# Optimization experiments

Hardware: AMD Instinct MI355X
Metric: run time of the kernel (lower is better)

## Reference

```python
import jax, jax.numpy as jnp
import numpy as np


def setup_inputs() -> dict:
    key = jax.random.key(0)
    k1, k2, k3 = jax.random.split(key, 3)
    B, H, S, D = 2, 8, 4096, 64
    queries = jax.random.normal(k1, (B, H, S, D), dtype=jnp.float32)
    keys = jax.random.normal(k2, (B, H, S, D), dtype=jnp.float32)
    values = jax.random.normal(k3, (B, H, S, D), dtype=jnp.float32)
    mask = jnp.zeros((1, 1, S, S), dtype=jnp.float32)
    return {"queries": queries, "keys": keys, "values": values, "d_k": D, "mask": mask}


def reference(queries, keys, values, d_k, mask):
    # scores: [B, H, Sq, Sk]
    scale = 1.0 / jnp.sqrt(jnp.asarray(d_k, dtype=queries.dtype))
    scores = jnp.einsum("bhqd,bhkd->bhqk", queries, keys) * scale
    scores = scores + (-1e9) * mask  # additive mask, broadcasts over B, H
    weights = jax.nn.softmax(scores, axis=-1)
    return jnp.einsum("bhqk,bhkd->bhqd", weights, values)
```

## Files before the change

### kernel.cpp

```cpp
#include <hip/hip_runtime.h>

#define S_LEN 4096
#define DHEAD 64
#define BQ    128
#define BK    64
#define NT    (S_LEN / BK)
#define KPAD  72
#define NBH   16
#define TILE_HALFS (BK * DHEAD)
#define WS_KV_HALFS ((size_t)NBH * NT * TILE_HALFS)

typedef __fp16   pk16x2 __attribute__((ext_vector_type(2)));
typedef _Float16 half4v __attribute__((ext_vector_type(4)));
typedef _Float16 half8  __attribute__((ext_vector_type(8)));
typedef float    f32x4  __attribute__((ext_vector_type(4)));

__device__ __forceinline__ void gl_lds16(const _Float16* g, _Float16* l) {
    __builtin_amdgcn_global_load_lds(
        (const __attribute__((address_space(1))) unsigned int*)g,
        (__attribute__((address_space(3))) unsigned int*)l, 16, 0, 0);
}

__global__ void mask_flag_kernel(const float4* __restrict__ mask, int* __restrict__ flag) {
    const long stride = 2048L * 256;
    long i = (long)blockIdx.x * 256 + threadIdx.x;
    int nz = 0;
    #pragma unroll
    for (int it = 0; it < 8; ++it) {
        float4 a = mask[i + it * stride];
        nz |= (a.x != 0.f) | (a.y != 0.f) | (a.z != 0.f) | (a.w != 0.f);
    }
    if (__any(nz)) {
        if ((threadIdx.x & 63) == 0) atomicOr(flag, 1);
    }
}

__global__ void conv_kernel(const float* __restrict__ Kg, const float* __restrict__ Vg,
                            const float* __restrict__ mask,
                            _Float16* __restrict__ wsK, _Float16* __restrict__ wsV,
                            int* __restrict__ flag) {
    const int tid  = threadIdx.x;
    const int tile = blockIdx.x;
    __shared__ __align__(16) _Float16 T[64][64];

    if (blockIdx.y == 0) {
        const float* Ksrc = Kg + (long)tile * TILE_HALFS;
        _Float16*    dst  = wsK + (long)tile * TILE_HALFS;
        #pragma unroll
        for (int it = 0; it < 2; ++it) {
            int m = tid + it * 256;
            int r = m >> 3, c = m & 7;
            const float4* s4 = (const float4*)(Ksrc + r * DHEAD + ((c ^ (r & 7)) << 3));
            float4 a = s4[0], b = s4[1];
            union { pk16x2 p[4]; half8 h; } u;
            u.p[0] = __builtin_amdgcn_cvt_pkrtz(a.x, a.y);
            u.p[1] = __builtin_amdgcn_cvt_pkrtz(a.z, a.w);
            u.p[2] = __builtin_amdgcn_cvt_pkrtz(b.x, b.y);
            u.p[3] = __builtin_amdgcn_cvt_pkrtz(b.z, b.w);
            *(half8*)(dst + m * 8) = u.h;
        }
    } else if (blockIdx.y == 1) {
        const float* Vsrc = Vg + (long)tile * TILE_HALFS;
        const int r  = tid >> 2;
        const int d0 = (tid & 3) << 4;
        const float4* s4 = (const float4*)(Vsrc + r * DHEAD + d0);
        float vv[16];
        *(float4*)&vv[0]  = s4[0];
        *(float4*)&vv[4]  = s4[1];
        *(float4*)&vv[8]  = s4[2];
        *(float4*)&vv[12] = s4[3];
        #pragma unroll
        for (int j = 0; j < 16; j += 2) {
            pk16x2 p = __builtin_amdgcn_cvt_pkrtz(vv[j], vv[j + 1]);
            T[d0 + j][r]     = *((_Float16*)&p);
            T[d0 + j + 1][r] = *((_Float16*)&p + 1);
        }
        __syncthreads();
        _Float16* dst = wsV + (long)tile * TILE_HALFS;
        #pragma unroll
        for (int it = 0; it < 2; ++it) {
            int m = tid + it * 256;
            int d = m >> 3, c = m & 7;
            *(half8*)(dst + m * 8) = *(const half8*)&T[d][(c ^ (d & 7)) << 3];
        }
    } else {
        const float4* m4 = (const float4*)mask;
        const long stride = 1024L * 256;
        long i = (long)blockIdx.x * 256 + tid;
        int nz = 0;
        #pragma unroll
        for (int it = 0; it < 16; ++it) {
            float4 a = m4[i + it * stride];
            nz |= (a.x != 0.f) | (a.y != 0.f) | (a.z != 0.f) | (a.w != 0.f);
        }
        if (__any(nz)) {
            if ((tid & 63) == 0) atomicOr(flag, 1);
        }
    }
}

__global__ __launch_bounds__(256, 2) void attn_ws_kernel(
    const float* __restrict__ Q, const _Float16* __restrict__ KW,
    const _Float16* __restrict__ VW, const int* __restrict__ dk,
    const float* __restrict__ mask, const int* __restrict__ maskflag,
    float* __restrict__ O)
{
    const int qt   = blockIdx.x;
    const int bh   = blockIdx.y;
    const int tid  = threadIdx.x;
    const int wave = tid >> 6;
    const int lane = tid & 63;
    const int l15  = lane & 15;
    const int quad = lane >> 4;
    const int sw   = (l15 & 7) << 3;
    const int rq8  = quad << 3;

    const long base = (long)bh * S_LEN * DHEAD;
    const float* Qh = Q + base;
    float*       Oh = O + base;
    const _Float16* gk = KW + (long)bh * (NT * TILE_HALFS);
    const _Float16* gv = VW + (long)bh * (NT * TILE_HALFS);

    const int q0 = qt * BQ + wave * 32;
    const float csq  = rsqrtf((float)dk[0]) * 1.44269504088896f;
    const float mfac = -1e9f * 1.44269504088896f;
    const bool use_mask = (maskflag[0] != 0);

    __shared__ __align__(16) _Float16 KT[2][TILE_HALFS];
    __shared__ __align__(16) _Float16 VT[2][TILE_HALFS];
    __shared__ __align__(16) _Float16 Pw[4][32][KPAD];

    half8 qf[2][2];
    #pragma unroll
    for (int f = 0; f < 2; ++f) {
        #pragma unroll
        for (int kc = 0; kc < 2; ++kc) {
            const float4* src = (const float4*)(Qh + (long)(q0 + f*16 + l15) * DHEAD + kc*32 + rq8);
            float4 a = src[0], b = src[1];
            union { pk16x2 p[4]; half8 h; } u;
            u.p[0] = __builtin_amdgcn_cvt_pkrtz(a.x*csq, a.y*csq);
            u.p[1] = __builtin_amdgcn_cvt_pkrtz(a.z*csq, a.w*csq);
            u.p[2] = __builtin_amdgcn_cvt_pkrtz(b.x*csq, b.y*csq);
            u.p[3] = __builtin_amdgcn_cvt_pkrtz(b.z*csq, b.w*csq);
            qf[f][kc] = u.h;
        }
    }

    auto stage = [&](int kt, int b) {
        const _Float16* k8 = gk + (long)kt * TILE_HALFS + tid * 8;
        const _Float16* v8 = gv + (long)kt * TILE_HALFS + tid * 8;
        gl_lds16(k8,        &KT[b][tid * 8]);
        gl_lds16(k8 + 2048, &KT[b][2048 + tid * 8]);
        gl_lds16(v8,        &VT[b][tid * 8]);
        gl_lds16(v8 + 2048, &VT[b][2048 + tid * 8]);
    };

    f32x4 o[2][4];
    #pragma unroll
    for (int f = 0; f < 2; ++f)
        #pragma unroll
        for (int dt = 0; dt < 4; ++dt) o[f][dt] = (f32x4){0.f, 0.f, 0.f, 0.f};
    float m_i[2] = {-INFINITY, -INFINITY};
    float l_i[2] = {0.0f, 0.0f};

    stage(0, 0);
    __syncthreads();

    for (int kt = 0; kt < NT; ++kt) {
        const int b = kt & 1;
        if (kt + 1 < NT) stage(kt + 1, b ^ 1);

        f32x4 st[2][4];
        #pragma unroll
        for (int f = 0; f < 2; ++f)
            #pragma unroll
            for (int nt = 0; nt < 4; ++nt) st[f][nt] = (f32x4){0.f,0.f,0.f,0.f};
        __builtin_amdgcn_s_setprio(1);
        #pragma unroll
        for (int nt = 0; nt < 4; ++nt) {
            const int rb = (nt << 10) + (l15 << 6);
            #pragma unroll
            for (int kc = 0; kc < 2; ++kc) {
                half8 af = *(const half8*)&KT[b][rb + ((kc*32 + rq8) ^ sw)];
                st[0][nt] = __builtin_amdgcn_mfma_f32_16x16x32_f16(af, qf[0][kc], st[0][nt], 0, 0, 0);
                st[1][nt] = __builtin_amdgcn_mfma_f32_16x16x32_f16(af, qf[1][kc], st[1][nt], 0, 0, 0);
            }
        }
        __builtin_amdgcn_s_setprio(0);

        if (use_mask) {
            #pragma unroll
            for (int f = 0; f < 2; ++f) {
                const long mrow = (long)(q0 + f*16 + l15) * S_LEN + kt*BK;
                #pragma unroll
                for (int nt = 0; nt < 4; ++nt)
                    #pragma unroll
                    for (int r = 0; r < 4; ++r)
                        st[f][nt][r] += mfac * mask[mrow + nt*16 + quad*4 + r];
            }
        }

        #pragma unroll
        for (int f = 0; f < 2; ++f) {
            float mx = fmaxf(fmaxf(fmaxf(st[f][0][0], st[f][0][1]), fmaxf(st[f][0][2], st[f][0][3])),
                             fmaxf(fmaxf(st[f][1][0], st[f][1][1]), fmaxf(st[f][1][2], st[f][1][3])));
            float mx2 = fmaxf(fmaxf(fmaxf(st[f][2][0], st[f][2][1]), fmaxf(st[f][2][2], st[f][2][3])),
                              fmaxf(fmaxf(st[f][3][0], st[f][3][1]), fmaxf(st[f][3][2], st[f][3][3])));
            mx = fmaxf(mx, mx2);
            mx = fmaxf(mx, __shfl_xor(mx, 16, 64));
            mx = fmaxf(mx, __shfl_xor(mx, 32, 64));
            const bool need = __any(mx > m_i[f]);
            const float mnew = need ? fmaxf(m_i[f], mx) : m_i[f];
            float rsum = 0.0f;
            #pragma unroll
            for (int nt = 0; nt < 4; ++nt) {
                #pragma unroll
                for (int r = 0; r < 4; ++r) {
                    float p = __builtin_amdgcn_exp2f(st[f][nt][r] - mnew);
                    st[f][nt][r] = p;
                    rsum += p;
                }
            }
            rsum += __shfl_xor(rsum, 16, 64);
            rsum += __shfl_xor(rsum, 32, 64);
            if (need) {
                const float alpha = __builtin_amdgcn_exp2f(m_i[f] - mnew);
                #pragma unroll
                for (int r = 0; r < 4; ++r) {
                    float a_r = __shfl(alpha, quad*4 + r, 64);
                    #pragma unroll
                    for (int dt = 0; dt < 4; ++dt) o[f][dt][r] *= a_r;
                }
                l_i[f] = alpha * l_i[f] + rsum;
                m_i[f] = mnew;
            } else {
                l_i[f] += rsum;
            }
        }

        #pragma unroll
        for (int f = 0; f < 2; ++f)
            #pragma unroll
            for (int nt = 0; nt < 4; ++nt) {
                union { pk16x2 p[2]; half4v h; } up;
                up.p[0] = __builtin_amdgcn_cvt_pkrtz(st[f][nt][0], st[f][nt][1]);
                up.p[1] = __builtin_amdgcn_cvt_pkrtz(st[f][nt][2], st[f][nt][3]);
                *(half4v*)&Pw[wave][f*16 + l15][nt*16 + quad*4] = up.h;
            }

        __builtin_amdgcn_s_setprio(1);
        #pragma unroll
        for (int kc2 = 0; kc2 < 2; ++kc2) {
            half8 pa0 = *(const half8*)&Pw[wave][l15][kc2*32 + rq8];
            half8 pa1 = *(const half8*)&Pw[wave][16 + l15][kc2*32 + rq8];
            #pragma unroll
            for (int dt = 0; dt < 4; ++dt) {
                const int db = (dt << 10) + (l15 << 6);
                half8 vb = *(const half8*)&VT[b][db + ((kc2*32 + rq8) ^ sw)];
                o[0][dt] = __builtin_amdgcn_mfma_f32_16x16x32_f16(pa0, vb, o[0][dt], 0, 0, 0);
                o[1][dt] = __builtin_amdgcn_mfma_f32_16x16x32_f16(pa1, vb, o[1][dt], 0, 0, 0);
            }
        }
        __builtin_amdgcn_s_setprio(0);

        if (kt + 1 < NT) __syncthreads();
    }

    #pragma unroll
    for (int f = 0; f < 2; ++f) {
        #pragma unroll
        for (int r = 0; r < 4; ++r) {
            float lq = __shfl(l_i[f], quad*4 + r, 64);
            float linv = __builtin_amdgcn_rcpf(lq);
            const long row = (long)(q0 + f*16 + quad*4 + r) * DHEAD;
            #pragma unroll
            for (int dt = 0; dt < 4; ++dt)
                Oh[row + dt*16 + l15] = o[f][dt][r] * linv;
        }
    }
}

__global__ __launch_bounds__(256, 2) void attn_kernel_fb(
    const float* __restrict__ Q, const float* __restrict__ K,
    const float* __restrict__ V, const int* __restrict__ dk,
    const float* __restrict__ mask, const int* __restrict__ maskflag,
    float* __restrict__ O)
{
    const int qt   = blockIdx.x;
    const int bh   = blockIdx.y;
    const int tid  = threadIdx.x;
    const int wave = tid >> 6;
    const int lane = tid & 63;
    const int l15  = lane & 15;
    const int quad = lane >> 4;

    const long base = (long)bh * S_LEN * DHEAD;
    const float* Qh = Q + base;
    const float* Kh = K + base;
    const float* Vh = V + base;
    float*       Oh = O + base;

    const int q0 = qt * BQ + wave * 32;
    const float csq  = rsqrtf((float)dk[0]) * 1.44269504088896f;
    const float mfac = -1e9f * 1.44269504088896f;
    const bool use_mask = (maskflag[0] != 0);

    __shared__ __align__(16) _Float16 Kt[2][BK][KPAD];
    __shared__ __align__(16) _Float16 Vt[2][DHEAD * KPAD];
    __shared__ __align__(16) _Float16 Pw[4][32][KPAD];

    half8 qf[2][2];
    #pragma unroll
    for (int f = 0; f < 2; ++f) {
        #pragma unroll
        for (int kc = 0; kc < 2; ++kc) {
            const float4* src = (const float4*)(Qh + (long)(q0 + f*16 + l15) * DHEAD + kc*32 + quad*8);
            float4 a = src[0], b = src[1];
            union { pk16x2 p[4]; half8 h; } u;
            u.p[0] = __builtin_amdgcn_cvt_pkrtz(a.x*csq, a.y*csq);
            u.p[1] = __builtin_amdgcn_cvt_pkrtz(a.z*csq, a.w*csq);
            u.p[2] = __builtin_amdgcn_cvt_pkrtz(b.x*csq, b.y*csq);
            u.p[3] = __builtin_amdgcn_cvt_pkrtz(b.z*csq, b.w*csq);
            qf[f][kc] = u.h;
        }
    }

    const int kr  = tid >> 2;
    const int ks  = tid & 3;
    const int vrp = tid >> 3;
    const int vdq = tid & 7;
    const float* Kb = Kh + (long)kr * DHEAD + ks * 16;
    const float* Vb = Vh + (long)(2 * vrp) * DHEAD + vdq * 8;
    const int vcol = (((vrp >> 2) ^ vdq) << 3) + ((2 * vrp) & 7);
    const int vd0  = vdq * 8;

    float4 kf[4], vf[4];
    auto load_tile = [&](int kt) {
        const float4* kp  = (const float4*)(Kb + (long)kt * BK * DHEAD);
        kf[0] = kp[0]; kf[1] = kp[1]; kf[2] = kp[2]; kf[3] = kp[3];
        const float4* vp0 = (const float4*)(Vb + (long)kt * BK * DHEAD);
        const float4* vp1 = (const float4*)(Vb + (long)kt * BK * DHEAD + DHEAD);
        vf[0] = vp0[0]; vf[1] = vp0[1]; vf[2] = vp1[0]; vf[3] = vp1[1];
    };
    auto store_tile = [&](int b) {
        union { pk16x2 p[4]; half8 h; } u0, u1;
        u0.p[0] = __builtin_amdgcn_cvt_pkrtz(kf[0].x, kf[0].y);
        u0.p[1] = __builtin_amdgcn_cvt_pkrtz(kf[0].z, kf[0].w);
        u0.p[2] = __builtin_amdgcn_cvt_pkrtz(kf[1].x, kf[1].y);
        u0.p[3] = __builtin_amdgcn_cvt_pkrtz(kf[1].z, kf[1].w);
        u1.p[0] = __builtin_amdgcn_cvt_pkrtz(kf[2].x, kf[2].y);
        u1.p[1] = __builtin_amdgcn_cvt_pkrtz(kf[2].z, kf[2].w);
        u1.p[2] = __builtin_amdgcn_cvt_pkrtz(kf[3].x, kf[3].y);
        u1.p[3] = __builtin_amdgcn_cvt_pkrtz(kf[3].z, kf[3].w);
        *(half8*)&Kt[b][kr][ks*16]     = u0.h;
        *(half8*)&Kt[b][kr][ks*16 + 8] = u1.h;
        _Float16* vt = &Vt[b][0];
        *(pk16x2*)&vt[(vd0+0)*KPAD + vcol] = __builtin_amdgcn_cvt_pkrtz(vf[0].x, vf[2].x);
        *(pk16x2*)&vt[(vd0+1)*KPAD + vcol] = __builtin_amdgcn_cvt_pkrtz(vf[0].y, vf[2].y);
        *(pk16x2*)&vt[(vd0+2)*KPAD + vcol] = __builtin_amdgcn_cvt_pkrtz(vf[0].z, vf[2].z);
        *(pk16x2*)&vt[(vd0+3)*KPAD + vcol] = __builtin_amdgcn_cvt_pkrtz(vf[0].w, vf[2].w);
        *(pk16x2*)&vt[(vd0+4)*KPAD + vcol] = __builtin_amdgcn_cvt_pkrtz(vf[1].x, vf[3].x);
        *(pk16x2*)&vt[(vd0+5)*KPAD + vcol] = __builtin_amdgcn_cvt_pkrtz(vf[1].y, vf[3].y);
        *(pk16x2*)&vt[(vd0+6)*KPAD + vcol] = __builtin_amdgcn_cvt_pkrtz(vf[1].z, vf[3].z);
        *(pk16x2*)&vt[(vd0+7)*KPAD + vcol] = __builtin_amdgcn_cvt_pkrtz(vf[1].w, vf[3].w);
    };

    f32x4 o[2][4];
    #pragma unroll
    for (int f = 0; f < 2; ++f)
        #pragma unroll
        for (int dt = 0; dt < 4; ++dt) o[f][dt] = (f32x4){0.f, 0.f, 0.f, 0.f};
    float m_i[2] = {-INFINITY, -INFINITY};
    float l_i[2] = {0.0f, 0.0f};

    load_tile(0);
    store_tile(0);
    __syncthreads();

    for (int kt = 0; kt < NT; ++kt) {
        const int b = kt & 1;
        if (kt + 1 < NT) load_tile(kt + 1);

        f32x4 st[2][4];
        #pragma unroll
        for (int f = 0; f < 2; ++f)
            #pragma unroll
            for (int nt = 0; nt < 4; ++nt) st[f][nt] = (f32x4){0.f,0.f,0.f,0.f};
        #pragma unroll
        for (int nt = 0; nt < 4; ++nt) {
            #pragma unroll
            for (int kc = 0; kc < 2; ++kc) {
                half8 af = *(const half8*)&Kt[b][nt*16 + l15][kc*32 + quad*8];
                st[0][nt] = __builtin_amdgcn_mfma_f32_16x16x32_f16(af, qf[0][kc], st[0][nt], 0, 0, 0);
                st[1][nt] = __builtin_amdgcn_mfma_f32_16x16x32_f16(af, qf[1][kc], st[1][nt], 0, 0, 0);
            }
        }

        if (use_mask) {
            #pragma unroll
            for (int f = 0; f < 2; ++f) {
                const long mrow = (long)(q0 + f*16 + l15) * S_LEN + kt*BK;
                #pragma unroll
                for (int nt = 0; nt < 4; ++nt)
                    #pragma unroll
                    for (int r = 0; r < 4; ++r)
                        st[f][nt][r] += mfac * mask[mrow + nt*16 + quad*4 + r];
            }
        }

        float alpha[2];
        #pragma unroll
        for (int f = 0; f < 2; ++f) {
            float mx = fmaxf(fmaxf(fmaxf(st[f][0][0], st[f][0][1]), fmaxf(st[f][0][2], st[f][0][3])),
                             fmaxf(fmaxf(st[f][1][0], st[f][1][1]), fmaxf(st[f][1][2], st[f][1][3])));
            float mx2 = fmaxf(fmaxf(fmaxf(st[f][2][0], st[f][2][1]), fmaxf(st[f][2][2], st[f][2][3])),
                              fmaxf(fmaxf(st[f][3][0], st[f][3][1]), fmaxf(st[f][3][2], st[f][3][3])));
            mx = fmaxf(mx, mx2);
            mx = fmaxf(mx, __shfl_xor(mx, 16, 64));
            mx = fmaxf(mx, __shfl_xor(mx, 32, 64));
            float mnew = fmaxf(m_i[f], mx);
            float rsum = 0.0f;
            #pragma unroll
            for (int nt = 0; nt < 4; ++nt) {
                #pragma unroll
                for (int r = 0; r < 4; ++r) {
                    float p = __builtin_amdgcn_exp2f(st[f][nt][r] - mnew);
                    st[f][nt][r] = p;
                    rsum += p;
                }
            }
            rsum += __shfl_xor(rsum, 16, 64);
            rsum += __shfl_xor(rsum, 32, 64);
            alpha[f] = __builtin_amdgcn_exp2f(m_i[f] - mnew);
            l_i[f] = alpha[f] * l_i[f] + rsum;
            m_i[f] = mnew;
        }

        #pragma unroll
        for (int f = 0; f < 2; ++f)
            #pragma unroll
            for (int r = 0; r < 4; ++r) {
                float a_r = __shfl(alpha[f], quad*4 + r, 64);
                #pragma unroll
                for (int dt = 0; dt < 4; ++dt) o[f][dt][r] *= a_r;
            }

        #pragma unroll
        for (int f = 0; f < 2; ++f)
            #pragma unroll
            for (int nt = 0; nt < 4; ++nt) {
                union { pk16x2 p[2]; half4v h; } up;
                up.p[0] = __builtin_amdgcn_cvt_pkrtz(st[f][nt][0], st[f][nt][1]);
                up.p[1] = __builtin_amdgcn_cvt_pkrtz(st[f][nt][2], st[f][nt][3]);
                *(half4v*)&Pw[wave][f*16 + l15][nt*16 + quad*4] = up.h;
            }

        #pragma unroll
        for (int kc2 = 0; kc2 < 2; ++kc2) {
            half8 pa0 = *(const half8*)&Pw[wave][l15][kc2*32 + quad*8];
            half8 pa1 = *(const half8*)&Pw[wave][16 + l15][kc2*32 + quad*8];
            #pragma unroll
            for (int dt = 0; dt < 4; ++dt) {
                const int row = dt*16 + l15;
                const int pb  = (4*kc2 + quad) ^ (row >> 3);
                half8 vb = *(const half8*)&Vt[b][row*KPAD + pb*8];
                o[0][dt] = __builtin_amdgcn_mfma_f32_16x16x32_f16(pa0, vb, o[0][dt], 0, 0, 0);
                o[1][dt] = __builtin_amdgcn_mfma_f32_16x16x32_f16(pa1, vb, o[1][dt], 0, 0, 0);
            }
        }

        if (kt + 1 < NT) {
            store_tile((kt + 1) & 1);
            __syncthreads();
        }
    }

    #pragma unroll
    for (int f = 0; f < 2; ++f) {
        #pragma unroll
        for (int r = 0; r < 4; ++r) {
            float lq = __shfl(l_i[f], quad*4 + r, 64);
            float linv = __builtin_amdgcn_rcpf(lq);
            const long row = (long)(q0 + f*16 + quad*4 + r) * DHEAD;
            #pragma unroll
            for (int dt = 0; dt < 4; ++dt)
                Oh[row + dt*16 + l15] = o[f][dt][r] * linv;
        }
    }
}

extern "C" void kernel_launch(void* const* d_in, const int* in_sizes, int n_in,
                              void* d_out, int out_size, void* d_ws, size_t ws_size,
                              hipStream_t stream) {
    const float* Q    = (const float*)d_in[0];
    const float* K    = (const float*)d_in[1];
    const float* V    = (const float*)d_in[2];
    const int*   dk   = (const int*)d_in[3];
    const float* mask = (const float*)d_in[4];
    float* out = (float*)d_out;
    int* flag = (int*)d_ws;

    (void)hipMemsetAsync(flag, 0, sizeof(int), stream);

    const size_t WS_NEED = 256 + 2 * WS_KV_HALFS * sizeof(_Float16);
    dim3 grid(S_LEN / BQ, NBH);

    if (ws_size >= WS_NEED) {
        _Float16* wsK = (_Float16*)((char*)d_ws + 256);
        _Float16* wsV = wsK + WS_KV_HALFS;
        conv_kernel<<<dim3(NBH * NT, 3), 256, 0, stream>>>(K, V, mask, wsK, wsV, flag);
        attn_ws_kernel<<<grid, 256, 0, stream>>>(Q, wsK, wsV, dk, mask, flag, out);
    } else {
        mask_flag_kernel<<<2048, 256, 0, stream>>>((const float4*)mask, flag);
        attn_kernel_fb<<<grid, 256, 0, stream>>>(Q, K, V, dk, mask, flag, out);
    }
}
```

Before: 275.4 us.

## Halve per-wave query rows and raise occupancy in workspace attention kernel

Each wave now processes one 16-row query fragment instead of two, so blocks cover 64 queries and the grid doubles. Launch bounds rise to allow four blocks per CU, and the P staging buffer is shrunk and XOR-swizzled to avoid bank conflicts. The goal is better latency hiding through more resident waves. The cost is that each staged K/V tile is reused across half as many query rows, which increases LDS fill and load traffic per FLOP.

```diff
diff --git a/kernel.cpp b/kernel.cpp
--- a/kernel.cpp
+++ b/kernel.cpp
@@ -99,7 +99,7 @@
     }
 }
 
-__global__ __launch_bounds__(256, 2) void attn_ws_kernel(
+__global__ __launch_bounds__(256, 4) void attn_ws_kernel(
     const float* __restrict__ Q, const _Float16* __restrict__ KW,
     const _Float16* __restrict__ VW, const int* __restrict__ dk,
     const float* __restrict__ mask, const int* __restrict__ maskflag,
@@ -121,29 +121,26 @@
     const _Float16* gk = KW + (long)bh * (NT * TILE_HALFS);
     const _Float16* gv = VW + (long)bh * (NT * TILE_HALFS);
 
-    const int q0 = qt * BQ + wave * 32;
+    const int q0 = qt * 64 + wave * 16;
     const float csq  = rsqrtf((float)dk[0]) * 1.44269504088896f;
     const float mfac = -1e9f * 1.44269504088896f;
     const bool use_mask = (maskflag[0] != 0);
 
     __shared__ __align__(16) _Float16 KT[2][TILE_HALFS];
     __shared__ __align__(16) _Float16 VT[2][TILE_HALFS];
-    __shared__ __align__(16) _Float16 Pw[4][32][KPAD];
-
-    half8 qf[2][2];
-    #pragma unroll
-    for (int f = 0; f < 2; ++f) {
-        #pragma unroll
-        for (int kc = 0; kc < 2; ++kc) {
-            const float4* src = (const float4*)(Qh + (long)(q0 + f*16 + l15) * DHEAD + kc*32 + rq8);
-            float4 a = src[0], b = src[1];
-            union { pk16x2 p[4]; half8 h; } u;
-            u.p[0] = __builtin_amdgcn_cvt_pkrtz(a.x*csq, a.y*csq);
-            u.p[1] = __builtin_amdgcn_cvt_pkrtz(a.z*csq, a.w*csq);
-            u.p[2] = __builtin_amdgcn_cvt_pkrtz(b.x*csq, b.y*csq);
-            u.p[3] = __builtin_amdgcn_cvt_pkrtz(b.z*csq, b.w*csq);
-            qf[f][kc] = u.h;
-        }
+    __shared__ __align__(16) _Float16 Pw[4][16][64];
+
+    half8 qf[2];
+    #pragma unroll
+    for (int kc = 0; kc < 2; ++kc) {
+        const float4* src = (const float4*)(Qh + (long)(q0 + l15) * DHEAD + kc*32 + rq8);
+        float4 a = src[0], b = src[1];
+        union { pk16x2 p[4]; half8 h; } u;
+        u.p[0] = __builtin_amdgcn_cvt_pkrtz(a.x*csq, a.y*csq);
+        u.p[1] = __builtin_amdgcn_cvt_pkrtz(a.z*csq, a.w*csq);
+        u.p[2] = __builtin_amdgcn_cvt_pkrtz(b.x*csq, b.y*csq);
+        u.p[3] = __builtin_amdgcn_cvt_pkrtz(b.z*csq, b.w*csq);
+        qf[kc] = u.h;
     }
 
     auto stage = [&](int kt, int b) {
@@ -155,13 +152,11 @@
         gl_lds16(v8 + 2048, &VT[b][2048 + tid * 8]);
     };
 
-    f32x4 o[2][4];
-    #pragma unroll
-    for (int f = 0; f < 2; ++f)
-        #pragma unroll
-        for (int dt = 0; dt < 4; ++dt) o[f][dt] = (f32x4){0.f, 0.f, 0.f, 0.f};
-    float m_i[2] = {-INFINITY, -INFINITY};
-    float l_i[2] = {0.0f, 0.0f};
+    f32x4 o[4];
+    #pragma unroll
+    for (int dt = 0; dt < 4; ++dt) o[dt] = (f32x4){0.f, 0.f, 0.f, 0.f};
+    float m_i = -INFINITY;
+    float l_i = 0.0f;
 
     stage(0, 0);
     __syncthreads();
@@ -170,11 +165,9 @@
         const int b = kt & 1;
         if (kt + 1 < NT) stage(kt + 1, b ^ 1);
 
-        f32x4 st[2][4];
-        #pragma unroll
-        for (int f = 0; f < 2; ++f)
-            #pragma unroll
-            for (int nt = 0; nt < 4; ++nt) st[f][nt] = (f32x4){0.f,0.f,0.f,0.f};
+        f32x4 st[4];
+        #pragma unroll
+        for (int nt = 0; nt < 4; ++nt) st[nt] = (f32x4){0.f,0.f,0.f,0.f};
         __builtin_amdgcn_s_setprio(1);
         #pragma unroll
         for (int nt = 0; nt < 4; ++nt) {
@@ -182,83 +175,74 @@
             #pragma unroll
             for (int kc = 0; kc < 2; ++kc) {
                 half8 af = *(const half8*)&KT[b][rb + ((kc*32 + rq8) ^ sw)];
-                st[0][nt] = __builtin_amdgcn_mfma_f32_16x16x32_f16(af, qf[0][kc], st[0][nt], 0, 0, 0);
-                st[1][nt] = __builtin_amdgcn_mfma_f32_16x16x32_f16(af, qf[1][kc], st[1][nt], 0, 0, 0);
+                st[nt] = __builtin_amdgcn_mfma_f32_16x16x32_f16(af, qf[kc], st[nt], 0, 0, 0);
             }
         }
         __builtin_amdgcn_s_setprio(0);
 
         if (use_mask) {
-            #pragma unroll
-            for (int f = 0; f < 2; ++f) {
-                const long mrow = (long)(q0 + f*16 + l15) * S_LEN + kt*BK;
-                #pragma unroll
-                for (int nt = 0; nt < 4; ++nt)
-                    #pragma unroll
-                    for (int r = 0; r < 4; ++r)
-                        st[f][nt][r] += mfac * mask[mrow + nt*16 + quad*4 + r];
-            }
-        }
-
-        #pragma unroll
-        for (int f = 0; f < 2; ++f) {
-            float mx = fmaxf(fmaxf(fmaxf(st[f][0][0], st[f][0][1]), fmaxf(st[f][0][2], st[f][0][3])),
-                             fmaxf(fmaxf(st[f][1][0], st[f][1][1]), fmaxf(st[f][1][2], st[f][1][3])));
-            float mx2 = fmaxf(fmaxf(fmaxf(st[f][2][0], st[f][2][1]), fmaxf(st[f][2][2], st[f][2][3])),
-                              fmaxf(fmaxf(st[f][3][0], st[f][3][1]), fmaxf(st[f][3][2], st[f][3][3])));
+            const long mrow = (long)(q0 + l15) * S_LEN + kt*BK;
+            #pragma unroll
+            for (int nt = 0; nt < 4; ++nt)
+                #pragma unroll
+                for (int r = 0; r < 4; ++r)
+                    st[nt][r] += mfac * mask[mrow + nt*16 + quad*4 + r];
+        }
+
+        {
+            float mx = fmaxf(fmaxf(fmaxf(st[0][0], st[0][1]), fmaxf(st[0][2], st[0][3])),
+                             fmaxf(fmaxf(st[1][0], st[1][1]), fmaxf(st[1][2], st[1][3])));
+            float mx2 = fmaxf(fmaxf(fmaxf(st[2][0], st[2][1]), fmaxf(st[2][2], st[2][3])),
+                              fmaxf(fmaxf(st[3][0], st[3][1]), fmaxf(st[3][2], st[3][3])));
             mx = fmaxf(mx, mx2);
             mx = fmaxf(mx, __shfl_xor(mx, 16, 64));
             mx = fmaxf(mx, __shfl_xor(mx, 32, 64));
-            const bool need = __any(mx > m_i[f]);
-            const float mnew = need ? fmaxf(m_i[f], mx) : m_i[f];
+            const bool need = __any(mx > m_i);
+            const float mnew = need ? fmaxf(m_i, mx) : m_i;
             float rsum = 0.0f;
             #pragma unroll
             for (int nt = 0; nt < 4; ++nt) {
                 #pragma unroll
                 for (int r = 0; r < 4; ++r) {
-                    float p = __builtin_amdgcn_exp2f(st[f][nt][r] - mnew);
-                    st[f][nt][r] = p;
+                    float p = __builtin_amdgcn_exp2f(st[nt][r] - mnew);
+                    st[nt][r] = p;
                     rsum += p;
                 }
             }
             rsum += __shfl_xor(rsum, 16, 64);
             rsum += __shfl_xor(rsum, 32, 64);
             if (need) {
-                const float alpha = __builtin_amdgcn_exp2f(m_i[f] - mnew);
+                const float alpha = __builtin_amdgcn_exp2f(m_i - mnew);
                 #pragma unroll
                 for (int r = 0; r < 4; ++r) {
                     float a_r = __shfl(alpha, quad*4 + r, 64);
                     #pragma unroll
-                    for (int dt = 0; dt < 4; ++dt) o[f][dt][r] *= a_r;
+                    for (int dt = 0; dt < 4; ++dt) o[dt][r] *= a_r;
                 }
-                l_i[f] = alpha * l_i[f] + rsum;
-                m_i[f] = mnew;
+                l_i = alpha * l_i + rsum;
+                m_i = mnew;
             } else {
-                l_i[f] += rsum;
-            }
-        }
-
-        #pragma unroll
-        for (int f = 0; f < 2; ++f)
-            #pragma unroll
-            for (int nt = 0; nt < 4; ++nt) {
-                union { pk16x2 p[2]; half4v h; } up;
-                up.p[0] = __builtin_amdgcn_cvt_pkrtz(st[f][nt][0], st[f][nt][1]);
-                up.p[1] = __builtin_amdgcn_cvt_pkrtz(st[f][nt][2], st[f][nt][3]);
-                *(half4v*)&Pw[wave][f*16 + l15][nt*16 + quad*4] = up.h;
-            }
+                l_i += rsum;
+            }
+        }
+
+        #pragma unroll
+        for (int nt = 0; nt < 4; ++nt) {
+            union { pk16x2 p[2]; half4v h; } up;
+            up.p[0] = __builtin_amdgcn_cvt_pkrtz(st[nt][0], st[nt][1]);
+            up.p[1] = __builtin_amdgcn_cvt_pkrtz(st[nt][2], st[nt][3]);
+            *(half4v*)&Pw[wave][l15][(nt*16 + quad*4) ^ sw] = up.h;
+        }
 
         __builtin_amdgcn_s_setprio(1);
         #pragma unroll
         for (int kc2 = 0; kc2 < 2; ++kc2) {
-            half8 pa0 = *(const half8*)&Pw[wave][l15][kc2*32 + rq8];
-            half8 pa1 = *(const half8*)&Pw[wave][16 + l15][kc2*32 + rq8];
+            half8 pa = *(const half8*)&Pw[wave][l15][(kc2*32 + rq8) ^ sw];
             #pragma unroll
             for (int dt = 0; dt < 4; ++dt) {
                 const int db = (dt << 10) + (l15 << 6);
                 half8 vb = *(const half8*)&VT[b][db + ((kc2*32 + rq8) ^ sw)];
-                o[0][dt] = __builtin_amdgcn_mfma_f32_16x16x32_f16(pa0, vb, o[0][dt], 0, 0, 0);
-                o[1][dt] = __builtin_amdgcn_mfma_f32_16x16x32_f16(pa1, vb, o[1][dt], 0, 0, 0);
+                o[dt] = __builtin_amdgcn_mfma_f32_16x16x32_f16(pa, vb, o[dt], 0, 0, 0);
             }
         }
         __builtin_amdgcn_s_setprio(0);
@@ -267,16 +251,13 @@
     }
 
     #pragma unroll
-    for (int f = 0; f < 2; ++f) {
-        #pragma unroll
-        for (int r = 0; r < 4; ++r) {
-            float lq = __shfl(l_i[f], quad*4 + r, 64);
-            float linv = __builtin_amdgcn_rcpf(lq);
-            const long row = (long)(q0 + f*16 + quad*4 + r) * DHEAD;
-            #pragma unroll
-            for (int dt = 0; dt < 4; ++dt)
-                Oh[row + dt*16 + l15] = o[f][dt][r] * linv;
-        }
+    for (int r = 0; r < 4; ++r) {
+        float lq = __shfl(l_i, quad*4 + r, 64);
+        float linv = __builtin_amdgcn_rcpf(lq);
+        const long row = (long)(q0 + quad*4 + r) * DHEAD;
+        #pragma unroll
+        for (int dt = 0; dt < 4; ++dt)
+            Oh[row + dt*16 + l15] = o[dt][r] * linv;
     }
 }
 
@@ -503,15 +484,16 @@
     (void)hipMemsetAsync(flag, 0, sizeof(int), stream);
 
     const size_t WS_NEED = 256 + 2 * WS_KV_HALFS * sizeof(_Float16);
-    dim3 grid(S_LEN / BQ, NBH);
 
     if (ws_size >= WS_NEED) {
         _Float16* wsK = (_Float16*)((char*)d_ws + 256);
         _Float16* wsV = wsK + WS_KV_HALFS;
         conv_kernel<<<dim3(NBH * NT, 3), 256, 0, stream>>>(K, V, mask, wsK, wsV, flag);
+        dim3 grid(S_LEN / 64, NBH);
         attn_ws_kernel<<<grid, 256, 0, stream>>>(Q, wsK, wsV, dk, mask, flag, out);
     } else {
         mask_flag_kernel<<<2048, 256, 0, stream>>>((const float4*)mask, flag);
+        dim3 grid(S_LEN / BQ, NBH);
         attn_kernel_fb<<<grid, 256, 0, stream>>>(Q, K, V, dk, mask, flag, out);
     }
 }
```

Measured after the change: 263.7 us. -4.3%, faster.
